# Optimization experiments

Measured on AMD Instinct MI355X. Metric: run time of the kernel, lower is better.

## Reference

```python
import jax, jax.numpy as jnp
import numpy as np

B, T, D, H = 32, 8192, 128, 128

def setup_inputs() -> dict:
    key = jax.random.key(0)
    k1, k2, k3, k4, k5 = jax.random.split(key, 5)
    return {
        "encoder_outputs": jax.random.normal(k1, (B, T, D), dtype=jnp.float32),
        "decoder_hidden": jax.random.normal(k2, (B, H), dtype=jnp.float32),
        "W1": jax.random.normal(k3, (D, D), dtype=jnp.float32) * 0.08,
        "W2": jax.random.normal(k4, (H, D), dtype=jnp.float32) * 0.08,
        "V": jax.random.normal(k5, (D, 1), dtype=jnp.float32) * 0.08,
    }

def reference(encoder_outputs, decoder_hidden, W1, W2, V):
    # score: [B, T, D] = tanh(enc @ W1 + (dec @ W2)[:, None, :])
    score = jnp.tanh(jnp.einsum('btd,de->bte', encoder_outputs, W1)
                     + jnp.einsum('bh,hd->bd', decoder_hidden, W2)[:, None, :])
    # logits: [B, T, 1]; softmax over time axis (axis=1)
    logits = jnp.einsum('btd,do->bto', score, V)
    attention_weights = jax.nn.softmax(logits, axis=1)
    # context: [B, D] weighted sum over T
    context_vector = jnp.sum(attention_weights * encoder_outputs, axis=1)
    return context_vector, attention_weights
```

## Files before the change

### kernel.cpp

```cpp
#include <hip/hip_runtime.h>

#define B_ 32
#define T_ 8192
#define D_ 128
#define MBLK 128
#define NCHUNK 64

typedef __attribute__((ext_vector_type(8))) _Float16 half8;
typedef __attribute__((ext_vector_type(4))) _Float16 half4;
typedef __attribute__((ext_vector_type(4))) float floatx4;

__device__ __forceinline__ float tanh_fast(float x) {
    float e = __expf(2.0f * x);
    return 1.0f - __fdividef(2.0f, e + 1.0f);
}

__global__ void prep_kernel(const float* __restrict__ W1, half8* __restrict__ W1frag,
                            const float* __restrict__ dec, const float* __restrict__ W2,
                            float* __restrict__ bias) {
    int bid = blockIdx.x, tid = threadIdx.x;
    if (bid < 8) {
        int tg = bid * 256 + tid;
        int kk = tg >> 9, ni = (tg >> 6) & 7, lane = tg & 63;
        half8 h;
        #pragma unroll
        for (int j = 0; j < 8; ++j) {
            int k = kk * 32 + ((lane >> 4) * 8) + j;
            int n = ni * 16 + (lane & 15);
            h[j] = (_Float16)W1[k * 128 + n];
        }
        W1frag[tg] = h;
    } else {
        int b = (bid - 8) * 2 + (tid >> 7);
        int d = tid & 127;
        float acc = 0.f;
        for (int h = 0; h < 128; ++h)
            acc += dec[b * 128 + h] * W2[h * 128 + d];
        bias[b * 128 + d] = acc;
    }
}

__global__ __launch_bounds__(512)
void main_kernel(const float* __restrict__ enc, const half8* __restrict__ W1frag,
                 const float* __restrict__ bias, const float* __restrict__ V,
                 float* __restrict__ out_w, float* __restrict__ m_part,
                 float* __restrict__ s_part, float* __restrict__ c_part)
{
    __shared__ __align__(16) char smem_u[32768];
    __shared__ __align__(16) float red[MBLK];
    __shared__ __align__(16) float c_red[8][128];

    half8* bfr = (half8*)smem_u;
    char*  encl = smem_u;

    const int tid = threadIdx.x;
    const int l = tid & 63;
    const int w = tid >> 6;
    const int g = l >> 4;
    const int bid = blockIdx.x;
    const int b = bid >> 6;
    const int chunk = bid & 63;
    const int arow = w * 16 + (l & 15);
    const float* rowp = enc + ((long)b * T_ + (long)chunk * MBLK + arow) * D_ + g * 8;

    #pragma unroll
    for (int qi = 0; qi < 4; ++qi)
        __builtin_amdgcn_global_load_lds(
            (const __attribute__((address_space(1))) void*)(W1frag + qi * 512 + tid),
            (__attribute__((address_space(3))) void*)(bfr + qi * 512 + (w << 6)),
            16, 0, 0);

    __syncthreads();

    float4 f0[4], f1[4];
    #pragma unroll
    for (int kk = 0; kk < 4; ++kk) {
        f0[kk] = *(const float4*)(rowp + kk * 32);
        f1[kk] = *(const float4*)(rowp + kk * 32 + 4);
    }

    floatx4 acc[8];
    #pragma unroll
    for (int ni = 0; ni < 8; ++ni) acc[ni] = (floatx4)0.0f;

    half8 afr[4];
    #pragma unroll
    for (int kk = 0; kk < 4; ++kk) {
        half8 a;
        a[0] = (_Float16)f0[kk].x; a[1] = (_Float16)f0[kk].y;
        a[2] = (_Float16)f0[kk].z; a[3] = (_Float16)f0[kk].w;
        a[4] = (_Float16)f1[kk].x; a[5] = (_Float16)f1[kk].y;
        a[6] = (_Float16)f1[kk].z; a[7] = (_Float16)f1[kk].w;
        afr[kk] = a;
        #pragma unroll
        for (int ni = 0; ni < 8; ++ni)
            acc[ni] = __builtin_amdgcn_mfma_f32_16x16x32_f16(
                          bfr[(kk * 8 + ni) * 64 + l], afr[kk], acc[ni], 0, 0, 0);
    }

    __syncthreads();

    {
        const int asw = (arow & 7) << 4;
        #pragma unroll
        for (int kk = 0; kk < 4; ++kk) {
            int byte = arow * 256 + (((kk * 64) + (g * 16)) ^ asw);
            *(half8*)(encl + byte) = afr[kk];
        }
    }

    float lq = 0.f;
    #pragma unroll
    for (int ni = 0; ni < 8; ++ni) {
        float4 bf = *(const float4*)(bias + b * 128 + ni * 16 + g * 4);
        float4 vf = *(const float4*)(V + ni * 16 + g * 4);
        lq += tanh_fast(acc[ni][0] + bf.x) * vf.x;
        lq += tanh_fast(acc[ni][1] + bf.y) * vf.y;
        lq += tanh_fast(acc[ni][2] + bf.z) * vf.z;
        lq += tanh_fast(acc[ni][3] + bf.w) * vf.w;
    }
    lq += __shfl_xor(lq, 16);
    lq += __shfl_xor(lq, 32);
    if (l < 16) {
        red[w * 16 + l] = lq;
        out_w[(long)b * T_ + chunk * MBLK + w * 16 + l] = lq;
    }
    __syncthreads();

    float l0 = red[l], l1 = red[l + 64];
    float m = fmaxf(l0, l1);
    #pragma unroll
    for (int mk = 1; mk < 64; mk <<= 1) m = fmaxf(m, __shfl_xor(m, mk));
    {
        float s = __expf(l0 - m) + __expf(l1 - m);
        #pragma unroll
        for (int mk = 1; mk < 64; mk <<= 1) s += __shfl_xor(s, mk);
        if (tid == 0) {
            m_part[b * NCHUNK + chunk] = m;
            s_part[b * NCHUNK + chunk] = s;
        }
    }

    if (tid < 256) {
        const int rg = tid >> 5, dg = tid & 31;
        floatx4 cc = (floatx4)0.0f;
        #pragma unroll
        for (int rr = 0; rr < 16; ++rr) {
            int r = rg * 16 + rr;
            float wgt = __expf(red[r] - m);
            half4 h = *(const half4*)(encl + (r * 256 + ((dg * 8) ^ ((r & 7) << 4))));
            #pragma unroll
            for (int i = 0; i < 4; ++i) cc[i] += wgt * (float)h[i];
        }
        *(floatx4*)(&c_red[rg][dg * 4]) = cc;
    }
    __syncthreads();
    if (tid < 128) {
        float s = 0.f;
        #pragma unroll
        for (int gg = 0; gg < 8; ++gg) s += c_red[gg][tid];
        c_part[((long)b * NCHUNK + chunk) * 128 + tid] = s;
    }
}

__global__ __launch_bounds__(256)
void reduce_kernel(const float* __restrict__ m_part, const float* __restrict__ s_part,
                   const float* __restrict__ c_part, float* __restrict__ ctx,
                   float* __restrict__ mg, float* __restrict__ sginv)
{
    __shared__ float sc[64];
    __shared__ float stats[2];
    __shared__ float part[2][128];
    int b = blockIdx.x, tid = threadIdx.x;

    if (tid < 64) {
        float m = m_part[b * 64 + tid];
        float m_g = m;
        #pragma unroll
        for (int mk = 1; mk < 64; mk <<= 1) m_g = fmaxf(m_g, __shfl_xor(m_g, mk));
        float e = __expf(m - m_g);
        float s = s_part[b * 64 + tid] * e;
        #pragma unroll
        for (int mk = 1; mk < 64; mk <<= 1) s += __shfl_xor(s, mk);
        sc[tid] = e;
        if (tid == 0) {
            float inv = __fdividef(1.0f, s);
            stats[0] = m_g; stats[1] = inv;
            mg[b] = m_g; sginv[b] = inv;
        }
    }
    __syncthreads();
    float inv = stats[1];

    {
        int d = tid & 127, h = tid >> 7;
        float acc = 0.f;
        #pragma unroll 4
        for (int ch = h * 32; ch < h * 32 + 32; ++ch)
            acc += c_part[((long)b * 64 + ch) * 128 + d] * sc[ch];
        part[h][d] = acc;
    }
    __syncthreads();
    if (tid < 128)
        ctx[b * 128 + tid] = (part[0][tid] + part[1][tid]) * inv;
}

__global__ void finalize_kernel(float* __restrict__ out_w, const float* __restrict__ mg,
                                const float* __restrict__ sginv)
{
    int idx = blockIdx.x * 256 + threadIdx.x;
    int b = idx >> 13;
    float lg = out_w[idx];
    out_w[idx] = __expf(lg - mg[b]) * sginv[b];
}

extern "C" void kernel_launch(void* const* d_in, const int* in_sizes, int n_in,
                              void* d_out, int out_size, void* d_ws, size_t ws_size,
                              hipStream_t stream)
{
    const float* enc = (const float*)d_in[0];
    const float* dec = (const float*)d_in[1];
    const float* W1  = (const float*)d_in[2];
    const float* W2  = (const float*)d_in[3];
    const float* V   = (const float*)d_in[4];

    float* ctx  = (float*)d_out;
    float* outw = ctx + B_ * D_;

    float* ws     = (float*)d_ws;
    float* bias   = ws;
    float* m_part = bias + 4096;
    float* s_part = m_part + 2048;
    float* mg     = s_part + 2048;
    float* sginv  = mg + 32;
    float* c_part = sginv + 32;
    half8* W1frag = (half8*)(c_part + (long)B_ * NCHUNK * 128);

    prep_kernel<<<24, 256, 0, stream>>>(W1, W1frag, dec, W2, bias);
    main_kernel<<<B_ * NCHUNK, 512, 0, stream>>>(enc, W1frag, bias, V, outw, m_part, s_part, c_part);
    reduce_kernel<<<B_, 256, 0, stream>>>(m_part, s_part, c_part, ctx, mg, sginv);
    finalize_kernel<<<(B_ * T_) / 256, 256, 0, stream>>>(outw, mg, sginv);
}
```

Baseline: 56.67 us.

## Halve rows per block to 64 with 256 threads and double chunk count

Cuts each main-kernel block to 64 time rows and 256 threads, doubling the grid to 4096 blocks. The partial-softmax and context reduction are reworked to match, and the reduce kernel now combines 128 chunk partials through shared-memory tree reductions. The W1 fragment copy into LDS is moved ahead of the encoder loads so the barrier sits after both, letting them overlap. The aim is higher occupancy and better latency hiding. The cost is twice as many partial results to write and reduce, and every block still reloads the full 32 KB W1 tile, so that per-block load is now spread over half as many rows.

```diff
diff --git a/kernel.cpp b/kernel.cpp
--- a/kernel.cpp
+++ b/kernel.cpp
@@ -3,8 +3,8 @@
 #define B_ 32
 #define T_ 8192
 #define D_ 128
-#define MBLK 128
-#define NCHUNK 64
+#define MBLK 64
+#define NCHUNK 128
 
 typedef __attribute__((ext_vector_type(8))) _Float16 half8;
 typedef __attribute__((ext_vector_type(4))) _Float16 half4;
@@ -40,7 +40,7 @@
     }
 }
 
-__global__ __launch_bounds__(512)
+__global__ __launch_bounds__(256)
 void main_kernel(const float* __restrict__ enc, const half8* __restrict__ W1frag,
                  const float* __restrict__ bias, const float* __restrict__ V,
                  float* __restrict__ out_w, float* __restrict__ m_part,
@@ -58,19 +58,17 @@
     const int w = tid >> 6;
     const int g = l >> 4;
     const int bid = blockIdx.x;
-    const int b = bid >> 6;
-    const int chunk = bid & 63;
+    const int b = bid >> 7;
+    const int chunk = bid & 127;
     const int arow = w * 16 + (l & 15);
     const float* rowp = enc + ((long)b * T_ + (long)chunk * MBLK + arow) * D_ + g * 8;
 
     #pragma unroll
-    for (int qi = 0; qi < 4; ++qi)
+    for (int q = 0; q < 8; ++q)
         __builtin_amdgcn_global_load_lds(
-            (const __attribute__((address_space(1))) void*)(W1frag + qi * 512 + tid),
-            (__attribute__((address_space(3))) void*)(bfr + qi * 512 + (w << 6)),
+            (const __attribute__((address_space(1))) void*)(W1frag + q * 256 + tid),
+            (__attribute__((address_space(3))) void*)(bfr + q * 256 + (w << 6)),
             16, 0, 0);
-
-    __syncthreads();
 
     float4 f0[4], f1[4];
     #pragma unroll
@@ -78,6 +76,7 @@
         f0[kk] = *(const float4*)(rowp + kk * 32);
         f1[kk] = *(const float4*)(rowp + kk * 32 + 4);
     }
+    __syncthreads();
 
     floatx4 acc[8];
     #pragma unroll
@@ -127,12 +126,12 @@
     }
     __syncthreads();
 
-    float l0 = red[l], l1 = red[l + 64];
-    float m = fmaxf(l0, l1);
+    float lv = red[l];
+    float m = lv;
     #pragma unroll
     for (int mk = 1; mk < 64; mk <<= 1) m = fmaxf(m, __shfl_xor(m, mk));
     {
-        float s = __expf(l0 - m) + __expf(l1 - m);
+        float s = __expf(lv - m);
         #pragma unroll
         for (int mk = 1; mk < 64; mk <<= 1) s += __shfl_xor(s, mk);
         if (tid == 0) {
@@ -141,12 +140,12 @@
         }
     }
 
-    if (tid < 256) {
+    {
         const int rg = tid >> 5, dg = tid & 31;
         floatx4 cc = (floatx4)0.0f;
         #pragma unroll
-        for (int rr = 0; rr < 16; ++rr) {
-            int r = rg * 16 + rr;
+        for (int rr = 0; rr < 8; ++rr) {
+            int r = rg * 8 + rr;
             float wgt = __expf(red[r] - m);
             half4 h = *(const half4*)(encl + (r * 256 + ((dg * 8) ^ ((r & 7) << 4))));
             #pragma unroll
@@ -168,26 +167,32 @@
                    const float* __restrict__ c_part, float* __restrict__ ctx,
                    float* __restrict__ mg, float* __restrict__ sginv)
 {
-    __shared__ float sc[64];
+    __shared__ float sm[128];
+    __shared__ float sc[128];
     __shared__ float stats[2];
     __shared__ float part[2][128];
     int b = blockIdx.x, tid = threadIdx.x;
 
-    if (tid < 64) {
-        float m = m_part[b * 64 + tid];
-        float m_g = m;
-        #pragma unroll
-        for (int mk = 1; mk < 64; mk <<= 1) m_g = fmaxf(m_g, __shfl_xor(m_g, mk));
-        float e = __expf(m - m_g);
-        float s = s_part[b * 64 + tid] * e;
-        #pragma unroll
-        for (int mk = 1; mk < 64; mk <<= 1) s += __shfl_xor(s, mk);
-        sc[tid] = e;
-        if (tid == 0) {
-            float inv = __fdividef(1.0f, s);
-            stats[0] = m_g; stats[1] = inv;
-            mg[b] = m_g; sginv[b] = inv;
-        }
+    float m = 0.f;
+    if (tid < 128) { m = m_part[b * 128 + tid]; sm[tid] = m; }
+    __syncthreads();
+    for (int s = 64; s > 0; s >>= 1) {
+        if (tid < s) sm[tid] = fmaxf(sm[tid], sm[tid + s]);
+        __syncthreads();
+    }
+    float m_g = sm[0];
+    __syncthreads();
+    float e = 0.f;
+    if (tid < 128) { e = __expf(m - m_g); sm[tid] = s_part[b * 128 + tid] * e; sc[tid] = e; }
+    __syncthreads();
+    for (int s = 64; s > 0; s >>= 1) {
+        if (tid < s) sm[tid] += sm[tid + s];
+        __syncthreads();
+    }
+    if (tid == 0) {
+        float inv = __fdividef(1.0f, sm[0]);
+        stats[0] = m_g; stats[1] = inv;
+        mg[b] = m_g; sginv[b] = inv;
     }
     __syncthreads();
     float inv = stats[1];
@@ -196,8 +201,8 @@
         int d = tid & 127, h = tid >> 7;
         float acc = 0.f;
         #pragma unroll 4
-        for (int ch = h * 32; ch < h * 32 + 32; ++ch)
-            acc += c_part[((long)b * 64 + ch) * 128 + d] * sc[ch];
+        for (int ch = h * 64; ch < h * 64 + 64; ++ch)
+            acc += c_part[((long)b * 128 + ch) * 128 + d] * sc[ch];
         part[h][d] = acc;
     }
     __syncthreads();
@@ -230,14 +235,14 @@
     float* ws     = (float*)d_ws;
     float* bias   = ws;
     float* m_part = bias + 4096;
-    float* s_part = m_part + 2048;
-    float* mg     = s_part + 2048;
+    float* s_part = m_part + 4096;
+    float* mg     = s_part + 4096;
     float* sginv  = mg + 32;
     float* c_part = sginv + 32;
     half8* W1frag = (half8*)(c_part + (long)B_ * NCHUNK * 128);
 
     prep_kernel<<<24, 256, 0, stream>>>(W1, W1frag, dec, W2, bias);
-    main_kernel<<<B_ * NCHUNK, 512, 0, stream>>>(enc, W1frag, bias, V, outw, m_part, s_part, c_part);
+    main_kernel<<<B_ * NCHUNK, 256, 0, stream>>>(enc, W1frag, bias, V, outw, m_part, s_part, c_part);
     reduce_kernel<<<B_, 256, 0, stream>>>(m_part, s_part, c_part, ctx, mg, sginv);
     finalize_kernel<<<(B_ * T_) / 256, 256, 0, stream>>>(outw, mg, sginv);
 }
```

After: 56.65 us. About the same (-0.0%).
